# Kernel tuning notes

Hardware: AMD Instinct MI355X
Metric: run time of the kernel (lower is better)

## Reference

```python
import jax, jax.numpy as jnp
import numpy as np

B, S, D = 16, 2048, 128


def setup_inputs() -> dict:
    key = jax.random.key(0)
    kq, kk, kv = jax.random.split(key, 3)
    return {
        "queries": jax.random.normal(kq, (B, S, D), dtype=jnp.float32),
        "keys": jax.random.normal(kk, (B, S, D), dtype=jnp.float32),
        "values": jax.random.normal(kv, (B, S, D), dtype=jnp.float32),
        "mask": jnp.zeros((B, S, S), dtype=bool),  # True -> masked out
    }


def reference(queries, keys, values, mask):
    d_k = queries.shape[-1]
    scale = 1.0 / np.sqrt(d_k).astype(np.float32)
    # scores: [B, S, S]
    scores = jnp.einsum("bqd,bkd->bqk", queries, keys) * scale
    scores = jnp.where(mask, -jnp.inf, scores)
    attn_weights = jax.nn.softmax(scores, axis=-1)
    # dropout prob = 0.0 (eval), identity
    output = jnp.einsum("bqk,bkd->bqd", attn_weights, values)
    return output
```

## Files before the change

kernel.cpp:

```cpp
#include <hip/hip_runtime.h>
#include <hip/hip_bf16.h>

#define SEQ    2048
#define DIM    128
#define NBATCH 16
#define KVB    32
#define NSPLIT 4
#define QUART  (SEQ / NSPLIT)
#define NTILE  (QUART / KVB)
#define QW     32
#define NWAVE  4
#define QB     (QW * NWAVE)
#define NROW   (NBATCH * SEQ)
#define TELEM  (KVB * DIM)

typedef __bf16 bf16x8 __attribute__((ext_vector_type(8)));
typedef float  f32x16 __attribute__((ext_vector_type(16)));
typedef unsigned int uint;

#define LOG2E  1.44269504088896340736f
#define NEGINF (-__builtin_inff())

#define CVT_PK(d, lo, hi) asm("v_cvt_pk_bf16_f32 %0, %1, %2" : "=v"(d) : "v"(lo), "v"(hi))
#define SWAP32(x, y) asm("v_permlane32_swap_b32 %0, %1" : "+v"(x), "+v"(y))

typedef const __attribute__((address_space(1))) uint* gup;
typedef       __attribute__((address_space(3))) uint* lup;
#define GLDS16(g, l) __builtin_amdgcn_global_load_lds((gup)(g), (lup)(l), 16, 0, 0)

__global__ __launch_bounds__(256)
void sdpa_prep(const float* __restrict__ Kg, const float* __restrict__ Vg,
               __bf16* __restrict__ Kb, __bf16* __restrict__ Vb)
{
    const int tile = (int)blockIdx.x;
    const int tid  = (int)threadIdx.x;
    const size_t row0 = (size_t)tile * KVB;

    {
        const int kr = tid >> 3;
        const int c2 = (tid & 7) * 2;
        const int kx = kr & 7;
        const float* src = Kg + (row0 + kr) * DIM;
        __bf16* dst = Kb + (size_t)tile * TELEM + (size_t)kr * DIM;
        #pragma unroll
        for (int c = 0; c < 2; ++c) {
            const int ci = c2 + c;
            const int sc = ci ^ kx;
            const float4 a = *(const float4*)(src + sc * 8);
            const float4 b = *(const float4*)(src + sc * 8 + 4);
            bf16x8 h;
            h[0]=(__bf16)a.x; h[1]=(__bf16)a.y; h[2]=(__bf16)a.z; h[3]=(__bf16)a.w;
            h[4]=(__bf16)b.x; h[5]=(__bf16)b.y; h[6]=(__bf16)b.z; h[7]=(__bf16)b.w;
            *(bf16x8*)(dst + ci * 8) = h;
        }
    }
    {
        const int vd = tid & 127;
        const int cp = (tid >> 7) * 2;
        const int vx = (vd >> 1) & 3;
        const float* src = Vg + row0 * DIM + vd;
        __bf16* dst = Vb + (size_t)tile * TELEM + (size_t)vd * KVB;
        #pragma unroll
        for (int c = 0; c < 2; ++c) {
            const int ck = cp + c;
            const int ci = ck ^ vx;
            bf16x8 h;
            #pragma unroll
            for (int j = 0; j < 8; ++j) h[j] = (__bf16)src[(size_t)(ck * 8 + j) * DIM];
            *(bf16x8*)(dst + ci * 8) = h;
        }
    }
}

__global__ __launch_bounds__(256, 3)
void sdpa_main(const float* __restrict__ Qg, const __bf16* __restrict__ Kbf,
               const __bf16* __restrict__ Vbf, const unsigned char* __restrict__ Mg,
               float* __restrict__ Uw, float* __restrict__ Lw)
{
    __shared__ __bf16 Ksh[2][TELEM];
    __shared__ __bf16 Vsh[2][TELEM];

    const int tid  = (int)threadIdx.x;
    const int wid  = tid >> 6;
    const int lane = tid & 63;
    const int l31  = lane & 31;
    const int hi   = lane >> 5;
    const int kx7  = l31 & 7;
    const int vx3  = (l31 >> 1) & 3;

    const int bid  = (int)blockIdx.x;
    const int nbid = (bid & 7) * 128 + (bid >> 3);
    const int qtl  = nbid & 15;
    const int g    = nbid >> 4;
    const int quar = g & 3;
    const int bb   = g >> 2;
    const int q0w  = qtl * QB + wid * QW;

    const float qscale = 0.08838834764831845f * LOG2E;

    bf16x8 aq[8];
    {
        const float* qrow = Qg + ((size_t)(bb * SEQ + q0w + l31)) * DIM;
        #pragma unroll
        for (int m = 0; m < 8; ++m) {
            const float4 f0 = *(const float4*)(qrow + m * 16 + hi * 8);
            const float4 f1 = *(const float4*)(qrow + m * 16 + hi * 8 + 4);
            bf16x8 h;
            h[0] = (__bf16)(f0.x * qscale); h[1] = (__bf16)(f0.y * qscale);
            h[2] = (__bf16)(f0.z * qscale); h[3] = (__bf16)(f0.w * qscale);
            h[4] = (__bf16)(f1.x * qscale); h[5] = (__bf16)(f1.y * qscale);
            h[6] = (__bf16)(f1.z * qscale); h[7] = (__bf16)(f1.w * qscale);
            aq[m] = h;
        }
    }

    const __bf16* Kt0 = Kbf + (size_t)(bb * 64 + quar * 16) * TELEM;
    const __bf16* Vt0 = Vbf + (size_t)(bb * 64 + quar * 16) * TELEM;
    const unsigned char* Mrow = Mg + (size_t)bb * SEQ * SEQ
                              + (size_t)(q0w + l31) * SEQ + quar * QUART + 4 * hi;

    uint mn0, mn1, mn2, mn3;
    const int loff = lane * 16;

    auto issue = [&](int t, int b) {
        const char* Ks = (const char*)(Kt0 + (size_t)t * TELEM);
        const char* Vs = (const char*)(Vt0 + (size_t)t * TELEM);
        char* Kd = (char*)Ksh[b];
        char* Vd = (char*)Vsh[b];
        #pragma unroll
        for (int j = 0; j < 2; ++j) {
            const int o = wid * 1024 + j * 4096;
            GLDS16(Ks + o + loff, Kd + o);
            GLDS16(Vs + o + loff, Vd + o);
        }
        const unsigned char* ms = Mrow + t * KVB;
        mn0 = *(const uint*)(ms);
        mn1 = *(const uint*)(ms + 8);
        mn2 = *(const uint*)(ms + 16);
        mn3 = *(const uint*)(ms + 24);
    };

    issue(0, 0);

    f32x16 acc[4];
    #pragma unroll
    for (int i = 0; i < 4; ++i) acc[i] = (f32x16)(0.0f);
    float l_run = 0.0f;

    for (int t = 0; t < NTILE; ++t) {
        asm volatile("s_waitcnt vmcnt(0)" ::: "memory");
        __syncthreads();
        const uint mw0 = mn0, mw1 = mn1, mw2 = mn2, mw3 = mn3;
        if (t + 1 < NTILE) issue(t + 1, (t + 1) & 1);

        const bf16x8* const Kc = (const bf16x8*)Ksh[t & 1];
        const bf16x8* const Vc = (const bf16x8*)Vsh[t & 1];

        f32x16 s = (f32x16)(0.0f);
        __builtin_amdgcn_s_setprio(1);
        #pragma unroll
        for (int m = 0; m < 8; ++m) {
            const bf16x8 a = Kc[l31 * 16 + ((2 * m + hi) ^ kx7)];
            s = __builtin_amdgcn_mfma_f32_32x32x16_bf16(a, aq[m], s, 0, 0, 0);
        }
        __builtin_amdgcn_s_setprio(0);

        if (mw0) {
            if (mw0 & 0x000000ffu) s[0] = NEGINF;
            if (mw0 & 0x0000ff00u) s[1] = NEGINF;
            if (mw0 & 0x00ff0000u) s[2] = NEGINF;
            if (mw0 & 0xff000000u) s[3] = NEGINF;
        }
        if (mw1) {
            if (mw1 & 0x000000ffu) s[4] = NEGINF;
            if (mw1 & 0x0000ff00u) s[5] = NEGINF;
            if (mw1 & 0x00ff0000u) s[6] = NEGINF;
            if (mw1 & 0xff000000u) s[7] = NEGINF;
        }
        if (mw2) {
            if (mw2 & 0x000000ffu) s[8]  = NEGINF;
            if (mw2 & 0x0000ff00u) s[9]  = NEGINF;
            if (mw2 & 0x00ff0000u) s[10] = NEGINF;
            if (mw2 & 0xff000000u) s[11] = NEGINF;
        }
        if (mw3) {
            if (mw3 & 0x000000ffu) s[12] = NEGINF;
            if (mw3 & 0x0000ff00u) s[13] = NEGINF;
            if (mw3 & 0x00ff0000u) s[14] = NEGINF;
            if (mw3 & 0xff000000u) s[15] = NEGINF;
        }

        float ps = 0.0f;
        #pragma unroll
        for (int r = 0; r < 16; ++r) { s[r] = __builtin_amdgcn_exp2f(s[r]); ps += s[r]; }
        l_run += ps;

        uint w0, w1, w2, w3, w4, w5, w6, w7;
        CVT_PK(w0, s[0],  s[1]);  CVT_PK(w1, s[2],  s[3]);
        CVT_PK(w2, s[4],  s[5]);  CVT_PK(w3, s[6],  s[7]);
        CVT_PK(w4, s[8],  s[9]);  CVT_PK(w5, s[10], s[11]);
        CVT_PK(w6, s[12], s[13]); CVT_PK(w7, s[14], s[15]);
        SWAP32(w0, w2); SWAP32(w1, w3);
        SWAP32(w4, w6); SWAP32(w5, w7);
        union W { uint w[4]; bf16x8 v; } u0, u1;
        u0.w[0] = w0; u0.w[1] = w1; u0.w[2] = w2; u0.w[3] = w3;
        u1.w[0] = w4; u1.w[1] = w5; u1.w[2] = w6; u1.w[3] = w7;
        const bf16x8 pa0 = u0.v;
        const bf16x8 pa1 = u1.v;

        __builtin_amdgcn_s_setprio(1);
        #pragma unroll
        for (int c = 0; c < 4; ++c) {
            const int dd = (c * 32 + l31) * 4;
            const bf16x8 bv0 = Vc[dd + (hi ^ vx3)];
            acc[c] = __builtin_amdgcn_mfma_f32_32x32x16_bf16(pa0, bv0, acc[c], 0, 0, 0);
            const bf16x8 bv1 = Vc[dd + ((2 + hi) ^ vx3)];
            acc[c] = __builtin_amdgcn_mfma_f32_32x32x16_bf16(pa1, bv1, acc[c], 0, 0, 0);
        }
        __builtin_amdgcn_s_setprio(0);
    }

    l_run += __shfl_xor(l_run, 32);
    if (hi == 0)
        Lw[(size_t)quar * NROW + bb * SEQ + q0w + l31] = l_run;

    float* ub = Uw + ((size_t)quar * NROW + bb * SEQ + q0w) * DIM + l31;
    #pragma unroll
    for (int r = 0; r < 16; ++r) {
        const int q = (r & 3) + 8 * (r >> 2) + 4 * hi;
        #pragma unroll
        for (int c = 0; c < 4; ++c)
            ub[(size_t)q * DIM + c * 32] = acc[c][r];
    }
}

__global__ __launch_bounds__(256)
void sdpa_combine(float* __restrict__ Og, const float* __restrict__ Uw,
                  const float* __restrict__ Lw)
{
    const int gid = (int)blockIdx.x * 256 + (int)threadIdx.x;
    const int row = gid >> 5;
    const float inv = 1.0f / (Lw[row] + Lw[NROW + row]
                            + Lw[2 * NROW + row] + Lw[3 * (size_t)NROW + row]);
    const size_t slab = (size_t)NROW * DIM / 4;
    const float4* U = (const float4*)Uw;
    const float4 a = U[gid];
    const float4 b = U[slab + gid];
    const float4 c = U[2 * slab + gid];
    const float4 d = U[3 * slab + gid];
    float4 o;
    o.x = (a.x + b.x + c.x + d.x) * inv;
    o.y = (a.y + b.y + c.y + d.y) * inv;
    o.z = (a.z + b.z + c.z + d.z) * inv;
    o.w = (a.w + b.w + c.w + d.w) * inv;
    ((float4*)Og)[gid] = o;
}

extern "C" void kernel_launch(void* const* d_in, const int* in_sizes, int n_in,
                              void* d_out, int out_size, void* d_ws, size_t ws_size,
                              hipStream_t stream) {
    const float* Q = (const float*)d_in[0];
    const float* K = (const float*)d_in[1];
    const float* V = (const float*)d_in[2];
    const unsigned char* M = (const unsigned char*)d_in[3];
    float* O  = (float*)d_out;
    float*  Uw  = (float*)d_ws;
    float*  Lw  = Uw + (size_t)NSPLIT * NROW * DIM;
    __bf16* Kbf = (__bf16*)(Lw + (size_t)NSPLIT * NROW);
    __bf16* Vbf = Kbf + (size_t)NROW * DIM;
    sdpa_prep<<<dim3(NROW / KVB), dim3(256), 0, stream>>>(K, V, Kbf, Vbf);
    sdpa_main<<<dim3(NBATCH * 16 * NSPLIT), dim3(256), 0, stream>>>(Q, Kbf, Vbf, M, Uw, Lw);
    sdpa_combine<<<dim3(NROW * DIM / 4 / 256), dim3(256), 0, stream>>>(O, Uw, Lw);
}
```

Baseline: 92.37 us.

## Prefetch mask words two tiles ahead and relax the per-tile vmcnt wait

Result: slower. 101.9 us (+10.3%).

```diff
diff --git a/kernel.cpp b/kernel.cpp
--- a/kernel.cpp
+++ b/kernel.cpp
@@ -119,10 +119,9 @@
     const unsigned char* Mrow = Mg + (size_t)bb * SEQ * SEQ
                               + (size_t)(q0w + l31) * SEQ + quar * QUART + 4 * hi;
 
-    uint mn0, mn1, mn2, mn3;
     const int loff = lane * 16;
 
-    auto issue = [&](int t, int b) {
+    auto stage = [&](int t, int b) {
         const char* Ks = (const char*)(Kt0 + (size_t)t * TELEM);
         const char* Vs = (const char*)(Vt0 + (size_t)t * TELEM);
         char* Kd = (char*)Ksh[b];
@@ -133,25 +132,33 @@
             GLDS16(Ks + o + loff, Kd + o);
             GLDS16(Vs + o + loff, Vd + o);
         }
+    };
+    auto mload = [&](int t, uint& m0, uint& m1, uint& m2, uint& m3) {
         const unsigned char* ms = Mrow + t * KVB;
-        mn0 = *(const uint*)(ms);
-        mn1 = *(const uint*)(ms + 8);
-        mn2 = *(const uint*)(ms + 16);
-        mn3 = *(const uint*)(ms + 24);
+        m0 = *(const uint*)(ms);
+        m1 = *(const uint*)(ms + 8);
+        m2 = *(const uint*)(ms + 16);
+        m3 = *(const uint*)(ms + 24);
     };
-
-    issue(0, 0);
 
     f32x16 acc[4];
     #pragma unroll
     for (int i = 0; i < 4; ++i) acc[i] = (f32x16)(0.0f);
     float l_run = 0.0f;
 
-    for (int t = 0; t < NTILE; ++t) {
-        asm volatile("s_waitcnt vmcnt(0)" ::: "memory");
-        __syncthreads();
-        const uint mw0 = mn0, mw1 = mn1, mw2 = mn2, mw3 = mn3;
-        if (t + 1 < NTILE) issue(t + 1, (t + 1) & 1);
+    uint mA0, mA1, mA2, mA3;
+    uint mB0, mB1, mB2, mB3;
+
+    stage(0, 0);
+    mload(0, mA0, mA1, mA2, mA3);
+    mload(1, mB0, mB1, mB2, mB3);
+
+    auto tile = [&](int t, uint& M0, uint& M1, uint& M2, uint& M3) {
+        asm volatile("s_waitcnt vmcnt(4)" ::: "memory");
+        __builtin_amdgcn_s_barrier();
+        const uint mw0 = M0, mw1 = M1, mw2 = M2, mw3 = M3;
+        stage(t + 1 < NTILE ? t + 1 : NTILE - 1, (t + 1) & 1);
+        mload(t + 2 < NTILE ? t + 2 : NTILE - 1, M0, M1, M2, M3);
 
         const bf16x8* const Kc = (const bf16x8*)Ksh[t & 1];
         const bf16x8* const Vc = (const bf16x8*)Vsh[t & 1];
@@ -218,6 +225,12 @@
             acc[c] = __builtin_amdgcn_mfma_f32_32x32x16_bf16(pa1, bv1, acc[c], 0, 0, 0);
         }
         __builtin_amdgcn_s_setprio(0);
+    };
+
+    #pragma unroll 1
+    for (int t = 0; t < NTILE; t += 2) {
+        tile(t,     mA0, mA1, mA2, mA3);
+        tile(t + 1, mB0, mB1, mB2, mB3);
     }
 
     l_run += __shfl_xor(l_run, 32);
```
